# Kernel optimization log

Measured on AMD Instinct MI355X. Metric: run time of the kernel, lower is better.

Reference implementation:

```python
import jax, jax.numpy as jnp
import numpy as np

NUM_HEADS = 8
WIN = (7, 7)


def _window_setup(H, W, hw, ww):
    # replicates idx_map_pad / token_window / nearest-interpolated window_map
    pad_h = (hw - H % hw) % hw
    pad_w = (ww - W % ww) % ww
    H_pad, W_pad = H + pad_h, W + pad_w
    nh, nw = H_pad // hw, W_pad // ww
    idx_map = jnp.arange(H * W, dtype=jnp.int32).reshape(H, W)
    idx_map_pad = jnp.full((H_pad, W_pad), H * W, dtype=jnp.int32)
    idx_map_pad = idx_map_pad.at[pad_h // 2:pad_h // 2 + H, pad_w // 2:pad_w // 2 + W].set(idx_map)
    token_window = idx_map_pad.reshape(nh, hw, nw, ww).transpose(0, 2, 1, 3).reshape(nh * nw, hw * ww)
    # nearest upsample of arange(nh*nw).reshape(nh,nw) to (H_pad,W_pad) then crop:
    # H_pad divisible by hw, so nearest index = padded_coord // hw
    ys = (jnp.arange(H, dtype=jnp.int32) + pad_h // 2) // hw
    xs = (jnp.arange(W, dtype=jnp.int32) + pad_w // 2) // ww
    window_map = ys[:, None] * nw + xs[None, :]  # [H, W]
    return token_window, window_map, nh * nw


def _grid_idx(loc_orig, H, W, dtype):
    xy = 0.5 * (loc_orig + 1.0) * jnp.array([W, H], dtype=dtype) - 0.5
    xg = jnp.clip(jnp.round(xy[..., 0]).astype(jnp.int32), 0, W - 1)
    yg = jnp.clip(jnp.round(xy[..., 1]).astype(jnp.int32), 0, H - 1)
    return xg, yg


def _token2map(feat, loc_orig, idx_agg_src, H, W):
    # scatter-average token features onto the H*W grid. feat: [B,Ns,Cp] -> [B,H*W,Cp]
    B, N0 = idx_agg_src.shape
    xg, yg = _grid_idx(jax.lax.stop_gradient(loc_orig), H, W, feat.dtype)
    pix = yg * W + xg  # [B, N0]
    f0 = jnp.take_along_axis(feat, idx_agg_src[..., None], axis=1)  # [B,N0,Cp]
    bidx = jnp.broadcast_to(jnp.arange(B, dtype=jnp.int32)[:, None], (B, N0))
    mp = jnp.zeros((B, H * W, feat.shape[-1]), feat.dtype).at[bidx, pix].add(f0)
    cnt = jnp.zeros((B, H * W, 1), feat.dtype).at[bidx, pix].add(1.0)
    return mp / (cnt + 1e-6)


def _forward(x, loc_orig, idx_agg, agg_weight, x_source, idx_agg_source, conf_source,
             H, W, q_w, q_b, kv_w, kv_b, proj_w, proj_b):
    B, N, C = x.shape
    Ns = x_source.shape[1]
    N0 = idx_agg_source.shape[1]
    Hh = NUM_HEADS
    d = C // Hh
    scale = d ** -0.5
    hw, ww = WIN
    token_window, window_map, nWin = _window_setup(H, W, hw, ww)  # [nWin,K], [H,W]

    q = (x @ q_w + q_b).reshape(B, N, Hh, d).transpose(0, 2, 1, 3)  # [B,Hh,N,d]

    # --- window assignment (no-grad block in torch) ---
    if H * W == N and Ns == N and N == N0:
        idx_window = jnp.broadcast_to(window_map.reshape(1, N), (B, N))
    else:
        lo = jax.lax.stop_gradient(loc_orig)
        xg, yg = _grid_idx(lo, H, W, x.dtype)
        idx_tmp = window_map[yg, xg]  # [B,N0] window id per original position
        bidx = jnp.broadcast_to(jnp.arange(B, dtype=jnp.int32)[:, None], (B, N0))
        pw = jnp.zeros((B, N, nWin), x.dtype).at[bidx, idx_agg, idx_tmp].add(
            jax.lax.stop_gradient(agg_weight).reshape(B, N0))
        idx_window = jnp.argmax(pw, axis=-1)  # [B,N]
    idx_K = token_window[idx_window]  # [B,N,K] key-pixel ids (H*W == pad token)

    # --- token2map: rasterize source tokens (+conf) onto grid ---
    src = jnp.concatenate([x_source, conf_source], axis=-1)  # [B,Ns,C+1]
    smap = _token2map(src, loc_orig, idx_agg_source, H, W)  # [B,H*W,C+1]
    xs = smap[..., :C]
    cs = smap[..., C:]
    xs = jnp.concatenate([xs, jnp.zeros((B, 1, C), xs.dtype)], axis=1)  # pad token
    cs = jnp.concatenate([cs, jnp.full((B, 1, 1), -jnp.inf, cs.dtype)], axis=1)

    M = H * W + 1
    kv = (xs @ kv_w + kv_b).reshape(B, M, 2, Hh, d).transpose(2, 0, 3, 1, 4)
    k, v = kv[0], kv[1]  # [B,Hh,M,d]

    # gather K/V per query window (f_attn / f_weighted_sum)
    kg = jax.vmap(lambda kb, ib: kb[:, ib])(k, idx_K)  # [B,Hh,N,K,d]
    vg = jax.vmap(lambda vb, ib: vb[:, ib])(v, idx_K)  # [B,Hh,N,K,d]
    conf_g = jax.vmap(lambda cb, ib: cb[ib, 0])(cs, idx_K)  # [B,N,K]

    attn = jnp.einsum('bhnd,bhnkd->bhnk', q * scale, kg) + conf_g[:, None]
    attn = jax.nn.softmax(attn, axis=-1)
    out = jnp.einsum('bhnk,bhnkd->bhnd', attn, vg)
    out = out.transpose(0, 2, 1, 3).reshape(B, N, C)
    return out @ proj_w + proj_b


def setup_inputs() -> dict:
    key = jax.random.key(0)
    ks = jax.random.split(key, 10)
    B, N, C, N0, H, W = 4, 784, 384, 3136, 56, 56
    x = jax.random.normal(ks[0], (B, N, C), jnp.float32)
    loc_orig = jax.random.uniform(ks[1], (B, N0, 2), jnp.float32, -1.0, 1.0)
    idx_agg = jax.random.randint(ks[2], (B, N0), 0, N, dtype=jnp.int32)
    agg_weight = jax.random.uniform(ks[3], (B, N0, 1), jnp.float32)
    x_source = jax.random.normal(ks[4], (B, N, C), jnp.float32)
    idx_agg_source = jax.random.randint(ks[5], (B, N0), 0, N, dtype=jnp.int32)
    conf_source = jax.random.normal(ks[6], (B, N, 1), jnp.float32)
    q_w = jax.random.normal(ks[7], (C, C), jnp.float32) * 0.02
    q_b = jnp.zeros((C,), jnp.float32)
    kv_w = jax.random.normal(ks[8], (C, 2 * C), jnp.float32) * 0.02
    kv_b = jnp.zeros((2 * C,), jnp.float32)
    proj_w = jax.random.normal(ks[9], (C, C), jnp.float32) * 0.02
    proj_b = jnp.zeros((C,), jnp.float32)
    return {'x': x, 'loc_orig': loc_orig, 'idx_agg': idx_agg, 'agg_weight': agg_weight,
            'x_source': x_source, 'idx_agg_source': idx_agg_source, 'conf_source': conf_source,
            'H': H, 'W': W, 'q_w': q_w, 'q_b': q_b, 'kv_w': kv_w, 'kv_b': kv_b,
            'proj_w': proj_w, 'proj_b': proj_b}


def reference(x, loc_orig, idx_agg, agg_weight, x_source, idx_agg_source, conf_source,
              H, W, q_w, q_b, kv_w, kv_b, proj_w, proj_b):
    return _forward(x, loc_orig, idx_agg, agg_weight, x_source, idx_agg_source, conf_source,
                    H, W, q_w, q_b, kv_w, kv_b, proj_w, proj_b)
```

## Files before the change

kernel.cpp:

```cpp
#include <hip/hip_runtime.h>
#include <hip/hip_bf16.h>
#include <cstdint>
#include <type_traits>

constexpr int B    = 4;
constexpr int N    = 784;
constexpr int C    = 384;
constexpr int NH   = 8;
constexpr int D    = 48;
constexpr int Himg = 56;
constexpr int Wimg = 56;
constexpr int HW   = 3136;
constexpr int NSRC = 3136;
constexpr int NWIN = 64;
constexpr int KWIN = 49;
constexpr int KPAD = 56;
constexpr int C2   = 2 * C;
constexpr int CAP  = 24;

constexpr size_t OFF_PW      = 0;
constexpr size_t SZ_PW       = (size_t)B * N * NWIN;
constexpr size_t OFF_CSUM    = OFF_PW + SZ_PW;
constexpr size_t SZ_CSUM     = (size_t)B * HW;
constexpr size_t OFF_CNT     = OFF_CSUM + SZ_CSUM;
constexpr size_t SZ_CNT      = (size_t)B * HW;
constexpr size_t ZERO_FLOATS = OFF_CNT + SZ_CNT;
constexpr size_t OFF_SLOTS   = ZERO_FLOATS;
constexpr size_t SZ_SLOTS    = (size_t)B * HW * CAP;
constexpr size_t OFF_Q       = OFF_SLOTS + SZ_SLOTS;
constexpr size_t SZ_Q        = (size_t)B * N * C;
constexpr size_t OFF_IDXW    = OFF_Q + SZ_Q;
constexpr size_t SZ_IDXW     = (size_t)B * N;
constexpr size_t OFF_ATTNO   = OFF_IDXW + SZ_IDXW;
constexpr size_t SZ_ATTNO_F  = ((size_t)B * N * C + 1) / 2;
constexpr size_t OFF_KV_F    = OFF_ATTNO + SZ_ATTNO_F;
constexpr size_t SZ_KV_F     = ((size_t)B * HW * C2 + 1) / 2;
constexpr size_t OFF_ABF_F   = OFF_KV_F + SZ_KV_F;
constexpr size_t SZ_ABF_F    = ((size_t)B * HW * C + 1) / 2;
constexpr size_t MAIN_BYTES  = (OFF_ABF_F + SZ_ABF_F) * 4;
constexpr size_t OFF_KVWT_BYTE  = MAIN_BYTES;
constexpr size_t SZ_KVWT        = (size_t)C2 * C;
constexpr size_t OFF_QWT_BYTE   = OFF_KVWT_BYTE + SZ_KVWT * 2;
constexpr size_t SZ_QWT         = (size_t)C * C;
constexpr size_t OFF_PROJWT_BYTE= OFF_QWT_BYTE + SZ_QWT * 2;
constexpr size_t SZ_PROJWT      = (size_t)C * C;
constexpr size_t OFF_FLAG_BYTE  = OFF_PROJWT_BYTE + SZ_PROJWT * 2;
constexpr size_t OFF_XBF_BYTE   = OFF_FLAG_BYTE + 16;
constexpr size_t SZ_XBF         = (size_t)B * N * C;
constexpr size_t WS_BYTES_NEEDED = OFF_XBF_BYTE + SZ_XBF * 2;

typedef __attribute__((ext_vector_type(8))) short bf16x8;
typedef __attribute__((ext_vector_type(8))) unsigned short u16x8;
typedef __attribute__((ext_vector_type(4))) float f32x4;

__device__ __forceinline__ unsigned short f2bf_bits(float f) {
    __hip_bfloat16 h = __float2bfloat16(f);
    return *reinterpret_cast<unsigned short*>(&h);
}
__device__ __forceinline__ float bflo(unsigned w) { return __uint_as_float(w << 16); }
__device__ __forceinline__ float bfhi(unsigned w) { return __uint_as_float(w & 0xffff0000u); }
__device__ __forceinline__ float bfbits2f(unsigned short u) {
    return __uint_as_float(((unsigned)u) << 16);
}

__device__ __forceinline__ float ldin(const void* p, size_t i, bool f32) {
    if (f32) return ((const float*)p)[i];
    return __bfloat162float(((const __hip_bfloat16*)p)[i]);
}

__device__ __forceinline__ void grid_idx(float lx, float ly, int& xg, int& yg) {
    float xf = 0.5f * (lx + 1.0f) * (float)Wimg - 0.5f;
    float yf = 0.5f * (ly + 1.0f) * (float)Himg - 0.5f;
    int x = (int)rintf(xf);
    int y = (int)rintf(yf);
    xg = min(max(x, 0), Wimg - 1);
    yg = min(max(y, 0), Himg - 1);
}

__global__ __launch_bounds__(64) void sniff_kernel(const unsigned short* __restrict__ qw_bits,
                                                   int* __restrict__ flag) {
    int t = threadIdx.x;
    int cnt = 0;
    #pragma unroll
    for (int i = 0; i < 8; i++) {
        unsigned u = qw_bits[t * 8 + i];
        float v = __uint_as_float(u << 16);
        if (fabsf(v) > 4.0f) cnt++;
    }
    #pragma unroll
    for (int off = 32; off >= 1; off >>= 1) cnt += __shfl_xor(cnt, off);
    if (t == 0) *flag = (cnt > 8) ? 1 : 0;
}

__device__ __forceinline__ void do_transpose_tile(
    const void* __restrict__ W, unsigned short* __restrict__ Wt,
    int K, int Nn, int n0, int k0, bool f32, int t, float (*tile)[33])
{
    int tx = t & 31, ty = t >> 5;
    #pragma unroll
    for (int i = 0; i < 4; i++)
        tile[ty + i * 8][tx] = ldin(W, (size_t)(k0 + ty + i * 8) * Nn + (n0 + tx), f32);
    __syncthreads();
    #pragma unroll
    for (int i = 0; i < 4; i++)
        Wt[(size_t)(n0 + ty + i * 8) * K + (k0 + tx)] = f2bf_bits(tile[tx][ty + i * 8]);
}

constexpr int PREP_BLOCKS = 1801;
__global__ __launch_bounds__(256) void prep_kernel(
    const void* __restrict__ kv_w, unsigned short* __restrict__ kvwt,
    const void* __restrict__ q_w, unsigned short* __restrict__ qwt,
    const void* __restrict__ proj_w, unsigned short* __restrict__ projwt,
    const void* __restrict__ x, unsigned short* __restrict__ xbf,
    const void* __restrict__ loc, const int* __restrict__ idx_agg,
    const void* __restrict__ agg_w, const int* __restrict__ idx_agg_src,
    const void* __restrict__ conf_src,
    float* __restrict__ pw, float* __restrict__ csum, int* __restrict__ cnti,
    int* __restrict__ slots, const int* __restrict__ flagp)
{
    __shared__ float tile[32][33];
    const bool f32 = (*flagp != 0);
    const int bid = blockIdx.x, t = threadIdx.x;
    if (bid < 288) {
        int j = bid;
        do_transpose_tile(kv_w, kvwt, C, C2, (j % 24) * 32, (j / 24) * 32, f32, t, tile);
    } else if (bid < 432) {
        int j = bid - 288;
        do_transpose_tile(q_w, qwt, C, C, (j % 12) * 32, (j / 12) * 32, f32, t, tile);
    } else if (bid < 576) {
        int j = bid - 432;
        do_transpose_tile(proj_w, projwt, C, C, (j % 12) * 32, (j / 12) * 32, f32, t, tile);
    } else if (bid < 1752) {
        int i = (bid - 576) * 1024 + t * 4;
        #pragma unroll
        for (int j = 0; j < 4; j++)
            xbf[i + j] = f2bf_bits(ldin(x, i + j, f32));
    } else {
        int p = (bid - 1752) * 256 + t;
        if (p < B * NSRC) {
            int b = p / NSRC;
            float lx = ldin(loc, (size_t)p * 2 + 0, f32);
            float ly = ldin(loc, (size_t)p * 2 + 1, f32);
            int xg, yg; grid_idx(lx, ly, xg, yg);
            int pix = yg * Wimg + xg;
            size_t bp = (size_t)b * HW + pix;
            int s = idx_agg_src[p];
            int slot = atomicAdd(&cnti[bp], 1);
            if (slot < CAP) slots[bp * CAP + slot] = s;
            atomicAdd(&csum[bp], ldin(conf_src, (size_t)b * N + s, f32));
            int win = (yg / 7) * 8 + (xg / 7);
            int n = idx_agg[p];
            atomicAdd(&pw[((size_t)b * N + n) * NWIN + win], ldin(agg_w, p, f32));
        }
    }
}

__global__ __launch_bounds__(256) void gather_kernel(
    const void* __restrict__ x_source,
    const int* __restrict__ cnti, const int* __restrict__ slots,
    unsigned short* __restrict__ abf, const int* __restrict__ flagp)
{
    const bool f32 = (*flagp != 0);
    const int g = blockIdx.x * 4 + (threadIdx.x >> 6);
    const int lane = threadIdx.x & 63;
    const int cf = cnti[g];
    const float sc = 1.0f / ((float)cf + 1e-6f);
    const int cn = min(cf, CAP);
    const int bb = g / HW;
    float a[6] = {0.f, 0.f, 0.f, 0.f, 0.f, 0.f};
    for (int si = 0; si < cn; si++) {
        int src = slots[(size_t)g * CAP + si];
        size_t off = ((size_t)bb * N + src) * C + lane * 6;
        if (f32) {
            const float* xr = (const float*)x_source + off;
            float4 v0 = *(const float4*)xr;
            float  v4 = xr[4], v5 = xr[5];
            a[0] += v0.x; a[1] += v0.y; a[2] += v0.z; a[3] += v0.w;
            a[4] += v4;   a[5] += v5;
        } else {
            const unsigned short* xr = (const unsigned short*)x_source + off;
            #pragma unroll
            for (int e = 0; e < 6; e++) a[e] += bfbits2f(xr[e]);
        }
    }
    unsigned short* dst = abf + (size_t)g * C + lane * 6;
    unsigned w0 = (unsigned)f2bf_bits(a[0] * sc) | ((unsigned)f2bf_bits(a[1] * sc) << 16);
    unsigned w1 = (unsigned)f2bf_bits(a[2] * sc) | ((unsigned)f2bf_bits(a[3] * sc) << 16);
    unsigned w2 = (unsigned)f2bf_bits(a[4] * sc) | ((unsigned)f2bf_bits(a[5] * sc) << 16);
    ((unsigned*)dst)[0] = w0;
    ((unsigned*)dst)[1] = w1;
    ((unsigned*)dst)[2] = w2;
}

constexpr int KV_BLOCKS = (C2 / 128) * ((B * HW) / 128);
constexpr int Q_BLOCKS  = (C / 128) * ((B * N + 127) / 128);
constexpr int AM_BLOCKS = (B * N + 255) / 256;
constexpr int MID_BLOCKS = KV_BLOCKS + Q_BLOCKS + AM_BLOCKS;
__global__ __launch_bounds__(256) void mid_kernel(
    const unsigned short* __restrict__ abf,
    const unsigned short* __restrict__ kvwt, const void* __restrict__ kv_b,
    unsigned short* __restrict__ kv_out,
    const unsigned short* __restrict__ xbf, const unsigned short* __restrict__ qwt,
    const void* __restrict__ q_b, float* __restrict__ q_out,
    const float* __restrict__ pw, int* __restrict__ idxw,
    const int* __restrict__ flagp, float scale)
{
    constexpr int SA = 40;
    __shared__ unsigned short As[128 * SA];
    __shared__ unsigned short Bs[128 * SA];
    const bool f32 = (*flagp != 0);
    const int bid = blockIdx.x;
    const int t = threadIdx.x;

    if (bid >= KV_BLOCKS + Q_BLOCKS) {
        int tt = (bid - KV_BLOCKS - Q_BLOCKS) * 256 + t;
        if (tt < B * N) {
            const float* row = pw + (size_t)tt * NWIN;
            float best = row[0]; int bi = 0;
            for (int j = 1; j < NWIN; j++) {
                float v = row[j];
                if (v > best) { best = v; bi = j; }
            }
            idxw[tt] = bi;
        }
        return;
    }

    const bool iskv = bid < KV_BLOCKS;
    const int j  = iskv ? bid : bid - KV_BLOCKS;
    const int nx = iskv ? (C2 / 128) : (C / 128);
    const int bn = (j % nx) * 128, bm = (j / nx) * 128;
    const int M  = iskv ? B * HW : B * N;
    const int Nn = iskv ? C2 : C;
    const int K  = C;
    const unsigned short* A  = iskv ? abf : xbf;
    const unsigned short* Bt = iskv ? kvwt : qwt;
    const void* bias = iskv ? kv_b : q_b;
    const float alpha = iskv ? 1.0f : scale;

    const int wave = t >> 6, lane = t & 63;
    const int quad = lane >> 4, l16 = lane & 15;
    const int wm = (wave >> 1) * 64, wn = (wave & 1) * 64;

    f32x4 acc[4][4] = {};

    for (int k0 = 0; k0 < K; k0 += 32) {
        #pragma unroll
        for (int ss = 0; ss < 2; ss++) {
            int s = t + ss * 256;
            int row = s >> 2, ch = s & 3;
            int grow = bm + row; if (grow >= M) grow = M - 1;
            *(u16x8*)&As[row * SA + ch * 8] =
                *(const u16x8*)(A + (size_t)grow * K + k0 + ch * 8);
            *(u16x8*)&Bs[row * SA + ch * 8] =
                *(const u16x8*)(Bt + (size_t)(bn + row) * K + k0 + ch * 8);
        }
        __syncthreads();

        bf16x8 af[4], bf[4];
        #pragma unroll
        for (int i = 0; i < 4; i++) {
            af[i] = *(const bf16x8*)&As[(wm + i * 16 + l16) * SA + quad * 8];
            bf[i] = *(const bf16x8*)&Bs[(wn + i * 16 + l16) * SA + quad * 8];
        }
        #pragma unroll
        for (int i = 0; i < 4; i++)
            #pragma unroll
            for (int jj = 0; jj < 4; jj++)
                acc[i][jj] = __builtin_amdgcn_mfma_f32_16x16x32_bf16(af[i], bf[jj], acc[i][jj], 0, 0, 0);
        __syncthreads();
    }

    #pragma unroll
    for (int i = 0; i < 4; i++) {
        int growb = bm + wm + i * 16 + quad * 4;
        #pragma unroll
        for (int jj = 0; jj < 4; jj++) {
            int gcol = bn + wn + jj * 16 + l16;
            float bv = ldin(bias, gcol, f32);
            #pragma unroll
            for (int r = 0; r < 4; r++) {
                int grow = growb + r;
                if (grow < M) {
                    float v = (acc[i][jj][r] + bv) * alpha;
                    size_t idx = (size_t)grow * Nn + gcol;
                    if (iskv) kv_out[idx] = f2bf_bits(v);
                    else      q_out[idx] = v;
                }
            }
        }
    }
}

__global__ __launch_bounds__(256) void mfma_gemm_kernel(
    const unsigned short* __restrict__ A,
    const unsigned short* __restrict__ Bt,
    const void* __restrict__ bias,
    void* __restrict__ Co,
    int M, int Nn, int K, float alpha, const int* __restrict__ flagp)
{
    constexpr int SA = 40;
    const bool f32 = (*flagp != 0);
    __shared__ unsigned short As[128 * SA];
    __shared__ unsigned short Bs[128 * SA];
    const int t = threadIdx.x;
    const int wave = t >> 6, lane = t & 63;
    const int quad = lane >> 4, l16 = lane & 15;
    const int wm = (wave >> 1) * 64, wn = (wave & 1) * 64;
    const int bm = blockIdx.y * 128, bn = blockIdx.x * 128;

    f32x4 acc[4][4] = {};

    for (int k0 = 0; k0 < K; k0 += 32) {
        #pragma unroll
        for (int ss = 0; ss < 2; ss++) {
            int s = t + ss * 256;
            int row = s >> 2, ch = s & 3;
            int grow = bm + row; if (grow >= M) grow = M - 1;
            *(u16x8*)&As[row * SA + ch * 8] =
                *(const u16x8*)(A + (size_t)grow * K + k0 + ch * 8);
            *(u16x8*)&Bs[row * SA + ch * 8] =
                *(const u16x8*)(Bt + (size_t)(bn + row) * K + k0 + ch * 8);
        }
        __syncthreads();

        bf16x8 af[4], bf[4];
        #pragma unroll
        for (int i = 0; i < 4; i++) {
            af[i] = *(const bf16x8*)&As[(wm + i * 16 + l16) * SA + quad * 8];
            bf[i] = *(const bf16x8*)&Bs[(wn + i * 16 + l16) * SA + quad * 8];
        }
        #pragma unroll
        for (int i = 0; i < 4; i++)
            #pragma unroll
            for (int j = 0; j < 4; j++)
                acc[i][j] = __builtin_amdgcn_mfma_f32_16x16x32_bf16(af[i], bf[j], acc[i][j], 0, 0, 0);
        __syncthreads();
    }

    #pragma unroll
    for (int i = 0; i < 4; i++) {
        int growb = bm + wm + i * 16 + quad * 4;
        #pragma unroll
        for (int j = 0; j < 4; j++) {
            int gcol = bn + wn + j * 16 + l16;
            float bv = ldin(bias, gcol, f32);
            #pragma unroll
            for (int r = 0; r < 4; r++) {
                int grow = growb + r;
                if (grow < M) {
                    float v = (acc[i][j][r] + bv) * alpha;
                    size_t idx = (size_t)grow * Nn + gcol;
                    if (f32) ((float*)Co)[idx] = v;
                    else     ((unsigned short*)Co)[idx] = f2bf_bits(v);
                }
            }
        }
    }
}

__global__ __launch_bounds__(512, 4) void attn_win_kernel(
    const float* __restrict__ q,
    const unsigned short* __restrict__ kv,
    const float* __restrict__ csum,
    const int* __restrict__ cnti,
    const int* __restrict__ idxw,
    unsigned short* __restrict__ attno)
{
    constexpr int SK  = 104;
    constexpr int SVT = 58;
    constexpr int CH  = 2 * D;
    __shared__ unsigned short s_k[KWIN * SK];
    __shared__ unsigned short s_vt[CH * SVT];
    __shared__ float s_p[8][KPAD];
    __shared__ unsigned short s_list[N];
    __shared__ float s_conf[KWIN];
    __shared__ int   s_cnt;

    const int t   = threadIdx.x;
    const int blk = blockIdx.x;
    const int b   = blk >> 8;
    const int win = (blk >> 2) & 63;
    const int par = blk & 3;
    const int wy = win >> 3, wx = win & 7;

    if (t == 0) s_cnt = 0;
    __syncthreads();
    for (int n = t; n < N; n += 512) {
        if (idxw[b * N + n] == win) {
            int slot = atomicAdd(&s_cnt, 1);
            s_list[slot] = (unsigned short)n;
        }
    }
    const unsigned* kvw = (const unsigned*)kv;
    for (int idx = t; idx < KWIN * (CH / 2); idx += 512) {
        int row = idx / (CH / 2), cw = idx % (CH / 2);
        int pix = (wy * 7 + row / 7) * Wimg + wx * 7 + row % 7;
        size_t gbase = ((size_t)b * HW + pix) * 384 + par * (CH / 2);
        *(unsigned*)&s_k[row * SK + cw * 2] = kvw[gbase + cw];
        unsigned vv = kvw[gbase + 192 + cw];
        int c0 = cw * 2;
        s_vt[(c0 + 0) * SVT + row] = (unsigned short)(vv & 0xffffu);
        s_vt[(c0 + 1) * SVT + row] = (unsigned short)(vv >> 16);
    }
    if (t < CH) {
        #pragma unroll
        for (int j = KWIN; j < KPAD; j++) s_vt[t * SVT + j] = 0;
    }
    if (t < KWIN) {
        int pix = (wy * 7 + t / 7) * Wimg + wx * 7 + t % 7;
        size_t bp = (size_t)b * HW + pix;
        s_conf[t] = csum[bp] / ((float)cnti[bp] + 1e-6f);
    }
    __syncthreads();

    const int cnt   = s_cnt;
    const int wave  = t >> 6;
    const int lane  = t & 63;
    const int hloc  = __builtin_amdgcn_readfirstlane(wave & 1);
    const int quart = wave >> 1;
    const int h     = par * 2 + hloc;

    if (lane >= KWIN && lane < KPAD) s_p[wave][lane] = 0.0f;

    const int krow = (lane < KWIN) ? lane : 0;
    uint4 kf[3];
    #pragma unroll
    for (int j = 0; j < 3; j++)
        kf[j] = *(const uint4*)&s_k[krow * SK + hloc * D + j * 16];
    const int dl = (lane < D) ? lane : 0;
    unsigned vw[28];
    {
        const unsigned short* vrow = &s_vt[(hloc * D + dl) * SVT];
        #pragma unroll
        for (int j = 0; j < 28; j++) vw[j] = *(const unsigned*)&vrow[j * 2];
    }
    const float confk = (lane < KWIN) ? s_conf[lane] : 0.0f;

    for (int ti = quart; ti < cnt; ti += 4) {
        const int n0 = __builtin_amdgcn_readfirstlane((int)s_list[ti]);
        const size_t bn = (size_t)b * N + n0;
        const float* qrow = q + bn * C + h * D;

        float l = -INFINITY;
        if (lane < KWIN) {
            float acc = confk;
            #pragma unroll
            for (int j = 0; j < 3; j++) {
                const int c = j * 16;
                acc += qrow[c +  0] * bflo(kf[j].x) + qrow[c +  1] * bfhi(kf[j].x);
                acc += qrow[c +  2] * bflo(kf[j].y) + qrow[c +  3] * bfhi(kf[j].y);
                acc += qrow[c +  4] * bflo(kf[j].z) + qrow[c +  5] * bfhi(kf[j].z);
                acc += qrow[c +  6] * bflo(kf[j].w) + qrow[c +  7] * bfhi(kf[j].w);
                uint4 k2 = *(const uint4*)&s_k[krow * SK + hloc * D + j * 16 + 8];
                acc += qrow[c +  8] * bflo(k2.x) + qrow[c +  9] * bfhi(k2.x);
                acc += qrow[c + 10] * bflo(k2.y) + qrow[c + 11] * bfhi(k2.y);
                acc += qrow[c + 12] * bflo(k2.z) + qrow[c + 13] * bfhi(k2.z);
                acc += qrow[c + 14] * bflo(k2.w) + qrow[c + 15] * bfhi(k2.w);
            }
            l = acc;
        }
        float m = l;
        #pragma unroll
        for (int off = 32; off >= 1; off >>= 1) m = fmaxf(m, __shfl_xor(m, off));
        float e = (lane < KWIN) ? expf(l - m) : 0.0f;
        float ssum = e;
        #pragma unroll
        for (int off = 32; off >= 1; off >>= 1) ssum += __shfl_xor(ssum, off);
        if (lane < KWIN) s_p[wave][lane] = e / ssum;
        __builtin_amdgcn_wave_barrier();

        float acc = 0.0f;
        const float4* pv4 = (const float4*)&s_p[wave][0];
        #pragma unroll
        for (int j = 0; j < KPAD / 4; j++) {
            float4 p4 = pv4[j];
            unsigned w0 = vw[j * 2], w1 = vw[j * 2 + 1];
            acc += p4.x * bflo(w0) + p4.y * bfhi(w0);
            acc += p4.z * bflo(w1) + p4.w * bfhi(w1);
        }
        if (lane < D) attno[bn * C + h * D + lane] = f2bf_bits(acc);
    }
}

extern "C" void kernel_launch(void* const* d_in, const int* in_sizes, int n_in,
                              void* d_out, int out_size, void* d_ws, size_t ws_size,
                              hipStream_t stream) {
    if (ws_size < WS_BYTES_NEEDED) return;

    const void* x        = d_in[0];
    const void* loc      = d_in[1];
    const int*  idx_agg  = (const int*)d_in[2];
    const void* agg_w    = d_in[3];
    const void* x_source = d_in[4];
    const int*  idx_asrc = (const int*)d_in[5];
    const void* conf_src = d_in[6];
    int wb = 9;
    if (!(n_in >= 15 && in_sizes[7] == 1 && in_sizes[8] == 1)) wb = 7;
    const void* q_w    = d_in[wb + 0];
    const void* q_b    = d_in[wb + 1];
    const void* kv_w   = d_in[wb + 2];
    const void* kv_b   = d_in[wb + 3];
    const void* proj_w = d_in[wb + 4];
    const void* proj_b = d_in[wb + 5];

    float* ws   = (float*)d_ws;
    float* pw   = ws + OFF_PW;
    float* csum = ws + OFF_CSUM;
    int*   cnti = (int*)(ws + OFF_CNT);
    int*   slots = (int*)(ws + OFF_SLOTS);
    float* q    = ws + OFF_Q;
    int*   idxw = (int*)(ws + OFF_IDXW);
    unsigned short* attno = (unsigned short*)(ws + OFF_ATTNO);
    unsigned short* kv  = (unsigned short*)(ws + OFF_KV_F);
    unsigned short* abf = (unsigned short*)(ws + OFF_ABF_F);
    unsigned short* kvwt   = (unsigned short*)((char*)d_ws + OFF_KVWT_BYTE);
    unsigned short* qwt    = (unsigned short*)((char*)d_ws + OFF_QWT_BYTE);
    unsigned short* projwt = (unsigned short*)((char*)d_ws + OFF_PROJWT_BYTE);
    int* flag = (int*)((char*)d_ws + OFF_FLAG_BYTE);
    unsigned short* xbf = (unsigned short*)((char*)d_ws + OFF_XBF_BYTE);

    sniff_kernel<<<1, 64, 0, stream>>>((const unsigned short*)q_w, flag);
    hipMemsetAsync(ws, 0, ZERO_FLOATS * sizeof(float), stream);
    prep_kernel<<<PREP_BLOCKS, 256, 0, stream>>>(
        kv_w, kvwt, q_w, qwt, proj_w, projwt, x, xbf,
        loc, idx_agg, agg_w, idx_asrc, conf_src,
        pw, csum, cnti, slots, flag);
    gather_kernel<<<B * HW / 4, 256, 0, stream>>>(x_source, cnti, slots, abf, flag);
    const float scale = (float)(1.0 / sqrt((double)D));
    mid_kernel<<<MID_BLOCKS, 256, 0, stream>>>(
        abf, kvwt, kv_b, kv, xbf, qwt, q_b, q, pw, idxw, flag, scale);
    attn_win_kernel<<<B * NWIN * 4, 512, 0, stream>>>(q, kv, csum, cnti, idxw, attno);
    mfma_gemm_kernel<<<dim3(C / 128, (B * N + 127) / 128), 256, 0, stream>>>(
        attno, projwt, proj_b, d_out, B * N, C, C, 1.0f, flag);

    (void)out_size;
}
```

Measured before the change: 198.8 us.

## Shrink mid-kernel GEMM row tile to 64 and regroup blocks by column tile

The fused KV/Q projection GEMM now uses 64x128 tiles instead of 128x128, which doubles the block count for better occupancy and load balance across CUs. Block indices are laid out column-tile-major with padded spans (200 and 56), so consecutive blocks share the same weight tile and improve L2 reuse; padding blocks exit early. The fp32 gather loop also switches from a float4 load to scalar loads, probably to avoid misaligned vector access at offsets of lane*6. The smaller tiles lower per-block arithmetic intensity and re-read the weight tiles more often.

```diff
diff --git a/kernel.cpp b/kernel.cpp
--- a/kernel.cpp
+++ b/kernel.cpp
@@ -173,10 +173,8 @@
         size_t off = ((size_t)bb * N + src) * C + lane * 6;
         if (f32) {
             const float* xr = (const float*)x_source + off;
-            float4 v0 = *(const float4*)xr;
-            float  v4 = xr[4], v5 = xr[5];
-            a[0] += v0.x; a[1] += v0.y; a[2] += v0.z; a[3] += v0.w;
-            a[4] += v4;   a[5] += v5;
+            #pragma unroll
+            for (int e = 0; e < 6; e++) a[e] += xr[e];
         } else {
             const unsigned short* xr = (const unsigned short*)x_source + off;
             #pragma unroll
@@ -192,10 +190,16 @@
     ((unsigned*)dst)[2] = w2;
 }
 
-constexpr int KV_BLOCKS = (C2 / 128) * ((B * HW) / 128);
-constexpr int Q_BLOCKS  = (C / 128) * ((B * N + 127) / 128);
+constexpr int KV_RT   = (B * HW) / 64;
+constexpr int KV_CT   = C2 / 128;
+constexpr int KV_SPAN = 200;
+constexpr int KV_REGION = KV_CT * KV_SPAN;
+constexpr int Q_RT    = (B * N) / 64;
+constexpr int Q_CT    = C / 128;
+constexpr int Q_SPAN  = 56;
+constexpr int Q_REGION = Q_CT * Q_SPAN;
 constexpr int AM_BLOCKS = (B * N + 255) / 256;
-constexpr int MID_BLOCKS = KV_BLOCKS + Q_BLOCKS + AM_BLOCKS;
+constexpr int MID_BLOCKS = KV_REGION + Q_REGION + AM_BLOCKS;
 __global__ __launch_bounds__(256) void mid_kernel(
     const unsigned short* __restrict__ abf,
     const unsigned short* __restrict__ kvwt, const void* __restrict__ kv_b,
@@ -206,14 +210,14 @@
     const int* __restrict__ flagp, float scale)
 {
     constexpr int SA = 40;
-    __shared__ unsigned short As[128 * SA];
+    __shared__ unsigned short As[64 * SA];
     __shared__ unsigned short Bs[128 * SA];
     const bool f32 = (*flagp != 0);
     const int bid = blockIdx.x;
     const int t = threadIdx.x;
 
-    if (bid >= KV_BLOCKS + Q_BLOCKS) {
-        int tt = (bid - KV_BLOCKS - Q_BLOCKS) * 256 + t;
+    if (bid >= KV_REGION + Q_REGION) {
+        int tt = (bid - KV_REGION - Q_REGION) * 256 + t;
         if (tt < B * N) {
             const float* row = pw + (size_t)tt * NWIN;
             float best = row[0]; int bi = 0;
@@ -226,10 +230,15 @@
         return;
     }
 
-    const bool iskv = bid < KV_BLOCKS;
-    const int j  = iskv ? bid : bid - KV_BLOCKS;
-    const int nx = iskv ? (C2 / 128) : (C / 128);
-    const int bn = (j % nx) * 128, bm = (j / nx) * 128;
+    bool iskv; int R, sct;
+    if (bid < KV_REGION) {
+        iskv = true;  sct = bid / KV_SPAN; R = bid % KV_SPAN;
+        if (R >= KV_RT) return;
+    } else {
+        iskv = false; int b2 = bid - KV_REGION; sct = b2 / Q_SPAN; R = b2 % Q_SPAN;
+        if (R >= Q_RT) return;
+    }
+    const int bm = R * 64, bn = sct * 128;
     const int M  = iskv ? B * HW : B * N;
     const int Nn = iskv ? C2 : C;
     const int K  = C;
@@ -240,31 +249,35 @@
 
     const int wave = t >> 6, lane = t & 63;
     const int quad = lane >> 4, l16 = lane & 15;
-    const int wm = (wave >> 1) * 64, wn = (wave & 1) * 64;
-
-    f32x4 acc[4][4] = {};
+    const int wm = (wave >> 1) * 32, wn = (wave & 1) * 64;
+
+    f32x4 acc[2][4] = {};
 
     for (int k0 = 0; k0 < K; k0 += 32) {
-        #pragma unroll
-        for (int ss = 0; ss < 2; ss++) {
-            int s = t + ss * 256;
-            int row = s >> 2, ch = s & 3;
+        {
+            int row = t >> 2, ch = t & 3;
             int grow = bm + row; if (grow >= M) grow = M - 1;
             *(u16x8*)&As[row * SA + ch * 8] =
                 *(const u16x8*)(A + (size_t)grow * K + k0 + ch * 8);
+        }
+        #pragma unroll
+        for (int ss = 0; ss < 2; ss++) {
+            int sI = t + ss * 256;
+            int row = sI >> 2, ch = sI & 3;
             *(u16x8*)&Bs[row * SA + ch * 8] =
                 *(const u16x8*)(Bt + (size_t)(bn + row) * K + k0 + ch * 8);
         }
         __syncthreads();
 
-        bf16x8 af[4], bf[4];
-        #pragma unroll
-        for (int i = 0; i < 4; i++) {
+        bf16x8 af[2], bf[4];
+        #pragma unroll
+        for (int i = 0; i < 2; i++)
             af[i] = *(const bf16x8*)&As[(wm + i * 16 + l16) * SA + quad * 8];
-            bf[i] = *(const bf16x8*)&Bs[(wn + i * 16 + l16) * SA + quad * 8];
-        }
-        #pragma unroll
-        for (int i = 0; i < 4; i++)
+        #pragma unroll
+        for (int j = 0; j < 4; j++)
+            bf[j] = *(const bf16x8*)&Bs[(wn + j * 16 + l16) * SA + quad * 8];
+        #pragma unroll
+        for (int i = 0; i < 2; i++)
             #pragma unroll
             for (int jj = 0; jj < 4; jj++)
                 acc[i][jj] = __builtin_amdgcn_mfma_f32_16x16x32_bf16(af[i], bf[jj], acc[i][jj], 0, 0, 0);
@@ -272,7 +285,7 @@
     }
 
     #pragma unroll
-    for (int i = 0; i < 4; i++) {
+    for (int i = 0; i < 2; i++) {
         int growb = bm + wm + i * 16 + quad * 4;
         #pragma unroll
         for (int jj = 0; jj < 4; jj++) {
```

Measured after the change: 186.4 us. -6.3%, faster.
